# Kernel optimization log

Hardware: AMD Instinct MI355X
Metric: run time of the kernel (lower is better)

## Reference

```python
import jax, jax.numpy as jnp
import numpy as np

NUM_EXPERTS = 3
INPUT_DIM = 1024
HIDDEN_DIM = 4096
OUTPUT_DIM = 1024
ROUTER_HIDDEN = 128
BATCH = 8192


def setup_inputs() -> dict:
    key = jax.random.key(0)
    ks = jax.random.split(key, 6)
    s_in = 1.0 / np.sqrt(INPUT_DIM)
    s_h = 1.0 / np.sqrt(HIDDEN_DIM)
    s_rh = 1.0 / np.sqrt(ROUTER_HIDDEN)
    return {
        "x": jax.random.normal(ks[0], (BATCH, INPUT_DIM), jnp.float32),
        "router_w1": jax.random.normal(ks[1], (INPUT_DIM, ROUTER_HIDDEN), jnp.float32) * s_in,
        "router_b1": jnp.zeros((ROUTER_HIDDEN,), jnp.float32),
        "router_w2": jax.random.normal(ks[2], (ROUTER_HIDDEN, NUM_EXPERTS), jnp.float32) * s_rh,
        "router_b2": jnp.zeros((NUM_EXPERTS,), jnp.float32),
        "expert_w1": jax.random.normal(ks[3], (NUM_EXPERTS, INPUT_DIM, HIDDEN_DIM), jnp.float32) * s_in,
        "expert_b1": jnp.zeros((NUM_EXPERTS, HIDDEN_DIM), jnp.float32),
        "expert_w2": jax.random.normal(ks[4], (NUM_EXPERTS, HIDDEN_DIM, OUTPUT_DIM), jnp.float32) * s_h,
        "expert_b2": jnp.zeros((NUM_EXPERTS, OUTPUT_DIM), jnp.float32),
    }


def reference(x, router_w1, router_b1, router_w2, router_b2,
              expert_w1, expert_b1, expert_w2, expert_b2):
    # Router: MLP -> softmax probs, hard top-1 selection (argmax)
    rh = jax.nn.relu(x @ router_w1 + router_b1)          # [B, 128]
    logits = rh @ router_w2 + router_b2                   # [B, E]
    probs = jax.nn.softmax(logits, axis=-1)
    selected = jnp.argmax(probs, axis=-1)                 # [B] int

    # Per-expert forward on all tokens (dense equivalent of masked dispatch)
    h = jax.nn.relu(jnp.einsum('bi,eih->ebh', x, expert_w1) + expert_b1[:, None, :])  # [E,B,H]
    y = jnp.einsum('ebh,eho->ebo', h, expert_w2) + expert_b2[:, None, :]              # [E,B,O]

    # Scatter-combine: each token takes its selected expert's output
    outputs = jnp.take_along_axis(
        y, selected[None, :, None], axis=0)[0]            # [B, O]

    # routing_stats: tokens per expert
    routing_stats = jnp.bincount(selected, length=NUM_EXPERTS)
    return outputs, routing_stats
```

## Files before the change

kernel.cpp:

```cpp
#include <hip/hip_runtime.h>
#include <hip/hip_bf16.h>

typedef short bf16x8 __attribute__((ext_vector_type(8)));
typedef float f32x4 __attribute__((ext_vector_type(4)));
typedef __attribute__((address_space(1))) const void gconst_t;
typedef __attribute__((address_space(3))) void lds_t;

#define DEVI __device__ __forceinline__

constexpr int BATCH   = 8192;
constexpr int IN_DIM  = 1024;
constexpr int HID     = 4096;
constexpr int OUT_DIM = 1024;
constexpr int NE      = 3;

constexpr size_t XBF_OFF  = 0;
constexpr size_t W1T_OFF  = 16777216;
constexpr size_t W2T_OFF  = W1T_OFF + 25165824;
constexpr size_t H_OFF    = W2T_OFF + 25165824;
constexpr size_t XLO_OFF  = H_OFF;
constexpr size_t RHP_OFF  = H_OFF + 16777216;
constexpr size_t META_OFF = H_OFF + 67108864;
constexpr size_t W3_OFF   = META_OFF + 131072;

DEVI unsigned short f2bf(float f) {
  __hip_bfloat16 h = __float2bfloat16(f);
  return *reinterpret_cast<unsigned short*>(&h);
}
DEVI float bf2f(unsigned short u) {
  unsigned v = (unsigned)u << 16;
  return __uint_as_float(v);
}

DEVI unsigned swz(unsigned b) { return b ^ (((b >> 7) & 7u) << 4); }

__global__ __launch_bounds__(256) void prepA_kernel(
    const float* __restrict__ x, const float* __restrict__ rw1,
    unsigned short* __restrict__ xb, unsigned short* __restrict__ xlo,
    unsigned short* __restrict__ w3) {
  __shared__ float tile[64][65];
  const int b = blockIdx.x;
  const int tid = threadIdx.x;
  if (b < 512) {
    const float4* xv4 = (const float4*)x;
    const int total = BATCH * IN_DIM / 4;
    for (int i = b * 256 + tid; i < total; i += 512 * 256) {
      const float4 v = xv4[i];
      ushort4 h, l;
      h.x = f2bf(v.x); l.x = f2bf(v.x - bf2f(h.x));
      h.y = f2bf(v.y); l.y = f2bf(v.y - bf2f(h.y));
      h.z = f2bf(v.z); l.z = f2bf(v.z - bf2f(h.z));
      h.w = f2bf(v.w); l.w = f2bf(v.w - bf2f(h.w));
      ((ushort4*)xb)[i] = h;
      ((ushort4*)xlo)[i] = l;
    }
  } else {
    const int w = b - 512;
    const int r0 = (w >> 1) * 64;
    const int c0 = (w & 1) * 64;
    const int tr = tid >> 4;
    const int tc = (tid & 15) << 2;
#pragma unroll
    for (int i = 0; i < 4; i++) {
      const int r = tr + i * 16;
      const float4 v = *(const float4*)(rw1 + (size_t)(r0 + r) * 128 + (c0 + tc));
      tile[r][tc + 0] = v.x; tile[r][tc + 1] = v.y; tile[r][tc + 2] = v.z; tile[r][tc + 3] = v.w;
    }
    __syncthreads();
#pragma unroll
    for (int i = 0; i < 4; i++) {
      const int c = tr + i * 16;
      ushort4 hi, lo;
      {
        float f;
        f = tile[tc + 0][c]; hi.x = f2bf(f); lo.x = f2bf(f - bf2f(hi.x));
        f = tile[tc + 1][c]; hi.y = f2bf(f); lo.y = f2bf(f - bf2f(hi.y));
        f = tile[tc + 2][c]; hi.z = f2bf(f); lo.z = f2bf(f - bf2f(hi.z));
        f = tile[tc + 3][c]; hi.w = f2bf(f); lo.w = f2bf(f - bf2f(hi.w));
      }
      unsigned short* base = w3 + (size_t)(c0 + c) * 3072 + (r0 + tc);
      *(ushort4*)(base)        = hi;
      *(ushort4*)(base + 1024) = hi;
      *(ushort4*)(base + 2048) = lo;
    }
  }
}

__global__ __launch_bounds__(256) void router_part(
    const unsigned short* __restrict__ xhi, const unsigned short* __restrict__ xlo,
    const unsigned short* __restrict__ w3, float* __restrict__ rhpart) {
  __shared__ unsigned short At[128 * 64];
  __shared__ unsigned short Bt[128 * 64];
  const int tid = threadIdx.x;
  const int m0 = blockIdx.x * 128;
  const int seg = blockIdx.y;
  const unsigned short* Abase = (seg == 1) ? xlo : xhi;
  const int kcol0 = seg * 1024;

  const unsigned short* asrc[4];
  const unsigned short* bsrc[4];
  unsigned loff[4];
#pragma unroll
  for (int l = 0; l < 4; l++) {
    const unsigned o = l * 4096u + (unsigned)tid * 16u;
    const unsigned p = swz(o);
    const int row = (int)(o >> 7);
    const int kel = (int)((p & 127u) >> 1);
    loff[l] = o;
    asrc[l] = Abase + (size_t)(m0 + row) * 1024 + kel;
    bsrc[l] = w3 + (size_t)row * 3072 + kcol0 + kel;
  }

  f32x4 acc[4][4];
#pragma unroll
  for (int i = 0; i < 4; i++)
#pragma unroll
    for (int j = 0; j < 4; j++) acc[i][j] = {0.f, 0.f, 0.f, 0.f};

  const int lane = tid & 63;
  const int wave = tid >> 6;
  const int wm = (wave >> 1) * 64;
  const int wn = (wave & 1) * 64;
  const int fr = lane & 15;
  const int fc = lane >> 4;

  for (int t = 0; t < 16; ++t) {
    __syncthreads();
#pragma unroll
    for (int l = 0; l < 4; l++) {
      __builtin_amdgcn_global_load_lds((gconst_t*)(asrc[l] + t * 64),
                                       (lds_t*)((char*)At + loff[l]), 16, 0, 0);
      __builtin_amdgcn_global_load_lds((gconst_t*)(bsrc[l] + t * 64),
                                       (lds_t*)((char*)Bt + loff[l]), 16, 0, 0);
    }
    __syncthreads();
    bf16x8 af[2][4], bv[2][4];
#pragma unroll
    for (int ks = 0; ks < 2; ks++) {
#pragma unroll
      for (int m = 0; m < 4; m++) {
        const unsigned L = (unsigned)(wm + m * 16 + fr) * 128u + (unsigned)(ks * 64 + fc * 16);
        af[ks][m] = *(const bf16x8*)((const char*)At + swz(L));
      }
#pragma unroll
      for (int n = 0; n < 4; n++) {
        const unsigned L = (unsigned)(wn + n * 16 + fr) * 128u + (unsigned)(ks * 64 + fc * 16);
        bv[ks][n] = *(const bf16x8*)((const char*)Bt + swz(L));
      }
    }
#pragma unroll
    for (int ks = 0; ks < 2; ks++)
#pragma unroll
      for (int m = 0; m < 4; m++)
#pragma unroll
        for (int n = 0; n < 4; n++)
          acc[m][n] = __builtin_amdgcn_mfma_f32_16x16x32_bf16(af[ks][m], bv[ks][n], acc[m][n], 0, 0, 0);
  }

  const int crow = (lane >> 4) * 4;
  const int ccol = lane & 15;
  float* outp = rhpart + (size_t)seg * BATCH * 128;
#pragma unroll
  for (int mi = 0; mi < 4; mi++) {
#pragma unroll
    for (int r = 0; r < 4; r++) {
      const int tok = m0 + wm + mi * 16 + crow + r;
#pragma unroll
      for (int ni = 0; ni < 4; ni++)
        outp[(size_t)tok * 128 + (wn + ni * 16 + ccol)] = acc[mi][ni][r];
    }
  }
}

__global__ __launch_bounds__(256) void router_finish(
    const float* __restrict__ rhpart, const float* __restrict__ rb1,
    const float* __restrict__ rw2, const float* __restrict__ rb2,
    int* __restrict__ counts, int* __restrict__ toklist) {
  __shared__ float rh[128 * 132];
  __shared__ float lg[128 * 3];
  const int tid = threadIdx.x;
  const int t0 = blockIdx.x * 128;
  constexpr size_t SEG = (size_t)BATCH * 128;

  for (int i = tid; i < 128 * 32; i += 256) {
    const int tok = i >> 5;
    const int c4 = (i & 31) * 4;
    const size_t base = (size_t)(t0 + tok) * 128 + c4;
    const float4 a = *(const float4*)(rhpart + base);
    const float4 b = *(const float4*)(rhpart + SEG + base);
    const float4 c = *(const float4*)(rhpart + 2 * SEG + base);
    const float4 bb = *(const float4*)(rb1 + c4);
    rh[tok * 132 + c4 + 0] = fmaxf(a.x + b.x + c.x + bb.x, 0.f);
    rh[tok * 132 + c4 + 1] = fmaxf(a.y + b.y + c.y + bb.y, 0.f);
    rh[tok * 132 + c4 + 2] = fmaxf(a.z + b.z + c.z + bb.z, 0.f);
    rh[tok * 132 + c4 + 3] = fmaxf(a.w + b.w + c.w + bb.w, 0.f);
  }
  __syncthreads();
#pragma unroll
  for (int pass = 0; pass < 2; ++pass) {
    const int t = tid + pass * 256;
    if (t < 384) {
      const int tok = t / 3, e = t - tok * 3;
      float s = rb2[e];
#pragma unroll 4
      for (int j = 0; j < 128; ++j) s = fmaf(rh[tok * 132 + j], rw2[j * 3 + e], s);
      lg[tok * 3 + e] = s;
    }
  }
  __syncthreads();
  if (tid < 128) {
    const float l0 = lg[tid * 3], l1 = lg[tid * 3 + 1], l2 = lg[tid * 3 + 2];
    int sel = 0; float m = l0;
    if (l1 > m) { m = l1; sel = 1; }
    if (l2 > m) { m = l2; sel = 2; }
    const int slot = atomicAdd(&counts[sel], 1);
    toklist[sel * BATCH + slot] = t0 + tid;
  }
}

__global__ __launch_bounds__(256) void prep2_kernel(
    const float* __restrict__ ew1, const float* __restrict__ ew2,
    unsigned short* __restrict__ w1t, unsigned short* __restrict__ w2t) {
  __shared__ float tile[64][65];
  const int b = blockIdx.x;
  const int tid = threadIdx.x;

  const float* src; unsigned short* dst; int R, C, r0, c0;
  if (b < 3072) {
    const int e = b / 1024, w = b % 1024;
    src = ew1 + (size_t)e * 1024 * 4096; dst = w1t + (size_t)e * 4096 * 1024;
    R = 1024; C = 4096; r0 = (w & 15) * 64; c0 = (w >> 4) * 64;
  } else {
    const int bb = b - 3072, e = bb / 1024, w = bb % 1024;
    src = ew2 + (size_t)e * 4096 * 1024; dst = w2t + (size_t)e * 1024 * 4096;
    R = 4096; C = 1024; r0 = (w & 63) * 64; c0 = (w >> 6) * 64;
  }
  const int tr = tid >> 4;
  const int tc = (tid & 15) << 2;
#pragma unroll
  for (int i = 0; i < 4; i++) {
    const int r = tr + i * 16;
    const float4 v = *(const float4*)(src + (size_t)(r0 + r) * C + (c0 + tc));
    tile[r][tc + 0] = v.x; tile[r][tc + 1] = v.y; tile[r][tc + 2] = v.z; tile[r][tc + 3] = v.w;
  }
  __syncthreads();
#pragma unroll
  for (int i = 0; i < 4; i++) {
    const int c = tr + i * 16;
    ushort4 o;
    o.x = f2bf(tile[tc + 0][c]);
    o.y = f2bf(tile[tc + 1][c]);
    o.z = f2bf(tile[tc + 2][c]);
    o.w = f2bf(tile[tc + 3][c]);
    *(ushort4*)(dst + (size_t)(c0 + c) * R + (r0 + tc)) = o;
  }
}

template <int MODE>
__global__ __launch_bounds__(256) void moe_gemm(
    const unsigned short* __restrict__ Abase, const unsigned short* __restrict__ Ball,
    const float* __restrict__ biasAll, unsigned short* __restrict__ Hout,
    float* __restrict__ Yout, const int* __restrict__ toklist, const int* __restrict__ counts,
    float* __restrict__ tail) {
  constexpr int N  = (MODE == 0) ? HID : OUT_DIM;
  constexpr int K  = (MODE == 0) ? IN_DIM : HID;
  constexpr int NT = K / 64;

  const int tid = threadIdx.x;
  if (MODE == 0 && blockIdx.x == 0 && blockIdx.y == 0 && tid < NE)
    tail[tid] = (float)counts[tid];

  const int c0 = counts[0], c1 = counts[1], c2 = counts[2];
  const int mb0 = (c0 + 127) >> 7, mb1 = (c1 + 127) >> 7, mb2 = (c2 + 127) >> 7;
  const int bx = blockIdx.x;
  int e, mblk;
  if (bx < mb0) { e = 0; mblk = bx; }
  else if (bx < mb0 + mb1) { e = 1; mblk = bx - mb0; }
  else if (bx < mb0 + mb1 + mb2) { e = 2; mblk = bx - mb0 - mb1; }
  else return;
  const int cnt = (e == 0) ? c0 : (e == 1) ? c1 : c2;
  const int m0 = mblk * 128;
  const int n0 = blockIdx.y * 128;
  const int off_e = (e > 0 ? c0 : 0) + (e > 1 ? c1 : 0);
  const unsigned short* Bmat = Ball + (size_t)e * ((size_t)N * K);
  const float* bias = biasAll + (size_t)e * N;

  __shared__ unsigned short At[128 * 64];
  __shared__ unsigned short Bt[128 * 64];

  const unsigned short* asrc[4];
  const unsigned short* bsrc[4];
  unsigned loff[4];
#pragma unroll
  for (int l = 0; l < 4; l++) {
    const unsigned o = l * 4096u + (unsigned)tid * 16u;
    const unsigned p = swz(o);
    const int row = (int)(o >> 7);
    const int kel = (int)((p & 127u) >> 1);
    loff[l] = o;
    int slot = m0 + row; if (slot > cnt - 1) slot = cnt - 1;
    const size_t arow = (MODE == 0) ? (size_t)toklist[e * BATCH + slot]
                                    : (size_t)(off_e + slot);
    asrc[l] = Abase + arow * K + kel;
    bsrc[l] = Bmat + (size_t)(n0 + row) * K + kel;
  }

  f32x4 acc[4][4];
#pragma unroll
  for (int i = 0; i < 4; i++)
#pragma unroll
    for (int j = 0; j < 4; j++) acc[i][j] = {0.f, 0.f, 0.f, 0.f};

  const int lane = tid & 63;
  const int wave = tid >> 6;
  const int wm = (wave >> 1) * 64;
  const int wn = (wave & 1) * 64;
  const int fr = lane & 15;
  const int fc = lane >> 4;

  for (int t = 0; t < NT; ++t) {
    __syncthreads();
#pragma unroll
    for (int l = 0; l < 4; l++) {
      __builtin_amdgcn_global_load_lds((gconst_t*)(asrc[l] + t * 64),
                                       (lds_t*)((char*)At + loff[l]), 16, 0, 0);
      __builtin_amdgcn_global_load_lds((gconst_t*)(bsrc[l] + t * 64),
                                       (lds_t*)((char*)Bt + loff[l]), 16, 0, 0);
    }
    __syncthreads();
    bf16x8 af[2][4], bv[2][4];
#pragma unroll
    for (int ks = 0; ks < 2; ks++) {
#pragma unroll
      for (int m = 0; m < 4; m++) {
        const unsigned L = (unsigned)(wm + m * 16 + fr) * 128u + (unsigned)(ks * 64 + fc * 16);
        af[ks][m] = *(const bf16x8*)((const char*)At + swz(L));
      }
#pragma unroll
      for (int n = 0; n < 4; n++) {
        const unsigned L = (unsigned)(wn + n * 16 + fr) * 128u + (unsigned)(ks * 64 + fc * 16);
        bv[ks][n] = *(const bf16x8*)((const char*)Bt + swz(L));
      }
    }
#pragma unroll
    for (int ks = 0; ks < 2; ks++)
#pragma unroll
      for (int m = 0; m < 4; m++)
#pragma unroll
        for (int n = 0; n < 4; n++)
          acc[m][n] = __builtin_amdgcn_mfma_f32_16x16x32_bf16(af[ks][m], bv[ks][n], acc[m][n], 0, 0, 0);
  }

  const int crow = (lane >> 4) * 4;
  const int ccol = lane & 15;
#pragma unroll
  for (int mi = 0; mi < 4; mi++) {
#pragma unroll
    for (int r = 0; r < 4; r++) {
      const int slot = m0 + wm + mi * 16 + crow + r;
      if (slot >= cnt) continue;
      if (MODE == 0) {
        unsigned short* hrow = Hout + (size_t)(off_e + slot) * HID;
#pragma unroll
        for (int ni = 0; ni < 4; ni++) {
          const int n = n0 + wn + ni * 16 + ccol;
          const float v = acc[mi][ni][r] + bias[n];
          hrow[n] = f2bf(fmaxf(v, 0.f));
        }
      } else {
        const int tok = toklist[e * BATCH + slot];
        float* yrow = Yout + (size_t)tok * OUT_DIM;
#pragma unroll
        for (int ni = 0; ni < 4; ni++) {
          const int n = n0 + wn + ni * 16 + ccol;
          yrow[n] = acc[mi][ni][r] + bias[n];
        }
      }
    }
  }
}

extern "C" void kernel_launch(void* const* d_in, const int* in_sizes, int n_in,
                              void* d_out, int out_size, void* d_ws, size_t ws_size,
                              hipStream_t stream) {
  const float* x   = (const float*)d_in[0];
  const float* rw1 = (const float*)d_in[1];
  const float* rb1 = (const float*)d_in[2];
  const float* rw2 = (const float*)d_in[3];
  const float* rb2 = (const float*)d_in[4];
  const float* ew1 = (const float*)d_in[5];
  const float* eb1 = (const float*)d_in[6];
  const float* ew2 = (const float*)d_in[7];
  const float* eb2 = (const float*)d_in[8];
  float* out = (float*)d_out;

  char* ws = (char*)d_ws;
  unsigned short* xb  = (unsigned short*)(ws + XBF_OFF);
  unsigned short* w1t = (unsigned short*)(ws + W1T_OFF);
  unsigned short* w2t = (unsigned short*)(ws + W2T_OFF);
  unsigned short* h   = (unsigned short*)(ws + H_OFF);
  unsigned short* xlo = (unsigned short*)(ws + XLO_OFF);
  float* rhpart = (float*)(ws + RHP_OFF);
  int* counts  = (int*)(ws + META_OFF);
  int* toklist = counts + 16;
  unsigned short* w3 = (unsigned short*)(ws + W3_OFF);
  float* tail = out + (size_t)BATCH * OUT_DIM;

  hipMemsetAsync(counts, 0, 64, stream);
  prepA_kernel<<<544, 256, 0, stream>>>(x, rw1, xb, xlo, w3);
  router_part<<<dim3(64, 3), 256, 0, stream>>>(xb, xlo, w3, rhpart);
  router_finish<<<64, 256, 0, stream>>>(rhpart, rb1, rw2, rb2, counts, toklist);
  prep2_kernel<<<6144, 256, 0, stream>>>(ew1, ew2, w1t, w2t);
  moe_gemm<0><<<dim3(66, 32), 256, 0, stream>>>(xb, w1t, eb1, h, nullptr, toklist, counts, tail);
  moe_gemm<1><<<dim3(66, 8), 256, 0, stream>>>(h, w2t, eb2, nullptr, out, toklist, counts, tail);
}
```

Before: 411.1 us.

## Triple-buffer MoE GEMM with 128x256 tiles and 512-thread blocks

Reworks the expert GEMM kernel to use 8 waves per block with a 128x256 output tile and a K-step of 32. Global-to-LDS loads run through a three-stage ring buffer, with manual vmcnt waits and a single barrier per iteration, so loads for step t+2 overlap MFMA work on step t. It also adds setprio around the MFMA block and a new XOR swizzle for the 64-byte rows. The cost is more LDS per block and finer K-steps, and the hand-placed waitcnt handling has to match the number of loads issued per stage.

```diff
diff --git a/kernel.cpp b/kernel.cpp
--- a/kernel.cpp
+++ b/kernel.cpp
@@ -257,14 +257,14 @@
 }
 
 template <int MODE>
-__global__ __launch_bounds__(256) void moe_gemm(
+__global__ __launch_bounds__(512, 2) void moe_gemm(
     const unsigned short* __restrict__ Abase, const unsigned short* __restrict__ Ball,
     const float* __restrict__ biasAll, unsigned short* __restrict__ Hout,
     float* __restrict__ Yout, const int* __restrict__ toklist, const int* __restrict__ counts,
     float* __restrict__ tail) {
   constexpr int N  = (MODE == 0) ? HID : OUT_DIM;
   constexpr int K  = (MODE == 0) ? IN_DIM : HID;
-  constexpr int NT = K / 64;
+  constexpr int NT = K / 32;
 
   const int tid = threadIdx.x;
   if (MODE == 0 && blockIdx.x == 0 && blockIdx.y == 0 && tid < NE)
@@ -280,28 +280,35 @@
   else return;
   const int cnt = (e == 0) ? c0 : (e == 1) ? c1 : c2;
   const int m0 = mblk * 128;
-  const int n0 = blockIdx.y * 128;
+  const int n0 = blockIdx.y * 256;
   const int off_e = (e > 0 ? c0 : 0) + (e > 1 ? c1 : 0);
   const unsigned short* Bmat = Ball + (size_t)e * ((size_t)N * K);
   const float* bias = biasAll + (size_t)e * N;
 
-  __shared__ unsigned short At[128 * 64];
-  __shared__ unsigned short Bt[128 * 64];
-
-  const unsigned short* asrc[4];
-  const unsigned short* bsrc[4];
-  unsigned loff[4];
-#pragma unroll
-  for (int l = 0; l < 4; l++) {
-    const unsigned o = l * 4096u + (unsigned)tid * 16u;
-    const unsigned p = swz(o);
-    const int row = (int)(o >> 7);
-    const int kel = (int)((p & 127u) >> 1);
-    loff[l] = o;
+  __shared__ unsigned short Ab[3][128 * 32];
+  __shared__ unsigned short Bb[3][256 * 32];
+
+  const unsigned short* asrc;
+  const unsigned short* bsrc[2];
+  unsigned aoff, boff[2];
+  {
+    const unsigned o = (unsigned)tid * 16u;
+    const unsigned p = o ^ (((o >> 6) & 3u) << 4);
+    const int row = (int)(o >> 6);
+    const int kel = (int)((p & 63u) >> 1);
+    aoff = o;
     int slot = m0 + row; if (slot > cnt - 1) slot = cnt - 1;
     const size_t arow = (MODE == 0) ? (size_t)toklist[e * BATCH + slot]
                                     : (size_t)(off_e + slot);
-    asrc[l] = Abase + arow * K + kel;
+    asrc = Abase + arow * K + kel;
+  }
+#pragma unroll
+  for (int l = 0; l < 2; l++) {
+    const unsigned o = l * 8192u + (unsigned)tid * 16u;
+    const unsigned p = o ^ (((o >> 6) & 3u) << 4);
+    const int row = (int)(o >> 6);
+    const int kel = (int)((p & 63u) >> 1);
+    boff[l] = o;
     bsrc[l] = Bmat + (size_t)(n0 + row) * K + kel;
   }
 
@@ -313,42 +320,57 @@
 
   const int lane = tid & 63;
   const int wave = tid >> 6;
-  const int wm = (wave >> 1) * 64;
-  const int wn = (wave & 1) * 64;
+  const int wm = (wave >> 2) * 64;
+  const int wn = (wave & 3) * 64;
   const int fr = lane & 15;
   const int fc = lane >> 4;
 
+  auto STAGE = [&](int buf, int kofs) {
+    __builtin_amdgcn_global_load_lds((gconst_t*)(asrc + kofs),
+                                     (lds_t*)((char*)&Ab[buf][0] + aoff), 16, 0, 0);
+#pragma unroll
+    for (int l = 0; l < 2; l++)
+      __builtin_amdgcn_global_load_lds((gconst_t*)(bsrc[l] + kofs),
+                                       (lds_t*)((char*)&Bb[buf][0] + boff[l]), 16, 0, 0);
+  };
+
+  STAGE(0, 0);
+  STAGE(1, 32);
+
+  int cur = 0;
   for (int t = 0; t < NT; ++t) {
-    __syncthreads();
-#pragma unroll
-    for (int l = 0; l < 4; l++) {
-      __builtin_amdgcn_global_load_lds((gconst_t*)(asrc[l] + t * 64),
-                                       (lds_t*)((char*)At + loff[l]), 16, 0, 0);
-      __builtin_amdgcn_global_load_lds((gconst_t*)(bsrc[l] + t * 64),
-                                       (lds_t*)((char*)Bt + loff[l]), 16, 0, 0);
-    }
-    __syncthreads();
-    bf16x8 af[2][4], bv[2][4];
-#pragma unroll
-    for (int ks = 0; ks < 2; ks++) {
-#pragma unroll
-      for (int m = 0; m < 4; m++) {
-        const unsigned L = (unsigned)(wm + m * 16 + fr) * 128u + (unsigned)(ks * 64 + fc * 16);
-        af[ks][m] = *(const bf16x8*)((const char*)At + swz(L));
-      }
-#pragma unroll
-      for (int n = 0; n < 4; n++) {
-        const unsigned L = (unsigned)(wn + n * 16 + fr) * 128u + (unsigned)(ks * 64 + fc * 16);
-        bv[ks][n] = *(const bf16x8*)((const char*)Bt + swz(L));
-      }
-    }
-#pragma unroll
-    for (int ks = 0; ks < 2; ks++)
-#pragma unroll
-      for (int m = 0; m < 4; m++)
-#pragma unroll
-        for (int n = 0; n < 4; n++)
-          acc[m][n] = __builtin_amdgcn_mfma_f32_16x16x32_bf16(af[ks][m], bv[ks][n], acc[m][n], 0, 0, 0);
+    if (t + 1 < NT) asm volatile("s_waitcnt vmcnt(3)" ::: "memory");
+    else            asm volatile("s_waitcnt vmcnt(0)" ::: "memory");
+    __builtin_amdgcn_sched_barrier(0);
+    __builtin_amdgcn_s_barrier();
+    __builtin_amdgcn_sched_barrier(0);
+    bf16x8 af[4], bv[4];
+#pragma unroll
+    for (int m = 0; m < 4; m++) {
+      const unsigned row = (unsigned)(wm + m * 16 + fr);
+      const unsigned addr = ((row << 6) + (unsigned)(fc << 4)) ^ ((row & 3u) << 4);
+      af[m] = *(const bf16x8*)((const char*)&Ab[cur][0] + addr);
+    }
+#pragma unroll
+    for (int n = 0; n < 4; n++) {
+      const unsigned row = (unsigned)(wn + n * 16 + fr);
+      const unsigned addr = ((row << 6) + (unsigned)(fc << 4)) ^ ((row & 3u) << 4);
+      bv[n] = *(const bf16x8*)((const char*)&Bb[cur][0] + addr);
+    }
+    asm volatile("s_waitcnt lgkmcnt(0)" ::: "memory");
+    __builtin_amdgcn_sched_barrier(0);
+    __builtin_amdgcn_s_setprio(1);
+#pragma unroll
+    for (int m = 0; m < 4; m++)
+#pragma unroll
+      for (int n = 0; n < 4; n++)
+        acc[m][n] = __builtin_amdgcn_mfma_f32_16x16x32_bf16(af[m], bv[n], acc[m][n], 0, 0, 0);
+    __builtin_amdgcn_s_setprio(0);
+    if (t + 2 < NT) {
+      const int nb = (cur + 2 >= 3) ? cur - 1 : cur + 2;
+      STAGE(nb, (t + 2) * 32);
+    }
+    cur = (cur + 1 == 3) ? 0 : cur + 1;
   }
 
   const int crow = (lane >> 4) * 4;
@@ -411,6 +433,6 @@
   router_part<<<dim3(64, 3), 256, 0, stream>>>(xb, xlo, w3, rhpart);
   router_finish<<<64, 256, 0, stream>>>(rhpart, rb1, rw2, rb2, counts, toklist);
   prep2_kernel<<<6144, 256, 0, stream>>>(ew1, ew2, w1t, w2t);
-  moe_gemm<0><<<dim3(66, 32), 256, 0, stream>>>(xb, w1t, eb1, h, nullptr, toklist, counts, tail);
-  moe_gemm<1><<<dim3(66, 8), 256, 0, stream>>>(h, w2t, eb2, nullptr, out, toklist, counts, tail);
-}
+  moe_gemm<0><<<dim3(66, 16), 512, 0, stream>>>(xb, w1t, eb1, h, nullptr, toklist, counts, tail);
+  moe_gemm<1><<<dim3(66, 4), 512, 0, stream>>>(h, w2t, eb2, nullptr, out, toklist, counts, tail);
+}
```

Measured after the change: 364.0 us. 1.13x faster.
